# Kernel tuning notes

Measured on AMD Instinct MI355X. Metric: run time of the kernel, lower is better.

The kernel has to match this reference:

```python
import jax, jax.numpy as jnp
import numpy as np

MAX_WAVELENGTH = 10000
BIG_NEG = -2.3819763e38


def _apply_rope(x, positions):
    """RoPE: positions [B,L] applied to x [B,L,H,D]."""
    d = x.shape[-1]
    freq_exponents = (2.0 / d) * jnp.arange(d // 2, dtype=jnp.float32)
    timescale = MAX_WAVELENGTH ** freq_exponents  # [D/2]
    radians = positions[..., None].astype(jnp.float32) / timescale  # [B,L,D/2]
    radians = radians[..., None, :]  # [B,L,1,D/2]
    sin, cos = jnp.sin(radians), jnp.cos(radians)
    x1, x2 = jnp.split(x, 2, axis=-1)
    return jnp.concatenate([x1 * cos - x2 * sin, x2 * cos + x1 * sin], axis=-1)


def setup_inputs() -> dict:
    key = jax.random.key(0)
    B, S, D, N, K, H = 2, 2048, 2048, 8, 1, 256  # batch, seq, features, q heads, kv heads, head_dim
    k1, k2, k3, k4 = jax.random.split(key, 4)
    x = jax.random.normal(k1, (B, S, D), dtype=jnp.float32)
    positions = jnp.broadcast_to(jnp.arange(S, dtype=jnp.int32), (B, S))
    attn_mask = jnp.tril(jnp.ones((S, S), dtype=bool))[None, None].repeat(B, axis=0)  # causal [B,1,S,S]
    q_w = jax.random.normal(k2, (N, D, H), dtype=jnp.float32) * (D ** -0.5)      # lecun_normal in_axis=-2
    kv_w = jax.random.normal(k3, (2, K, D, H), dtype=jnp.float32) * (D ** -0.5)
    out_w = jax.random.normal(k4, (N, H, D), dtype=jnp.float32) * (H ** -0.5)
    return {"x": x, "positions": positions, "attn_mask": attn_mask,
            "q_w": q_w, "kv_w": kv_w, "out_w": out_w}


def reference(x, positions, attn_mask, q_w, kv_w, out_w):
    B, T, D = x.shape
    N, _, H = q_w.shape
    K = kv_w.shape[1]
    G = N // K
    dtype = x.dtype

    q = jnp.einsum('btd,ndh->btnh', x, q_w)          # [B,T,N,H]
    kv = jnp.einsum('bsd,ckdh->cbskh', x, kv_w)      # [2,B,S,K,H]
    k, v = kv[0], kv[1]

    q = _apply_rope(q, positions) * (H ** -0.5)
    k = _apply_rope(k, positions)

    # prefill path: cache_size == S, so cache == k, v; idx = S
    qg = q.reshape(B, T, K, G, H)
    logits = jnp.einsum('btkgh,bskh->bkgts', qg, k,
                        preferred_element_type=jnp.float32)  # [B,K,G,T,S] fp32
    masked = jnp.where(attn_mask[:, :, None, :, :], logits, BIG_NEG)
    probs = jax.nn.softmax(masked, axis=-1).astype(dtype)
    enc = jnp.einsum('bkgts,bskh->btkgh', probs, v).reshape(B, T, N, H)
    out = jnp.einsum('btnh,nhd->btd', enc, out_w)
    return out
```

## Files before the change

### kernel.cpp

```cpp
#include <hip/hip_runtime.h>
#include <hip/hip_bf16.h>
#include <stdint.h>

#define BB 2
#define SS 2048
#define DD 2048
#define NHEAD 8
#define HH 256

typedef __bf16 bf16_t;
typedef __bf16 bf16x8 __attribute__((ext_vector_type(8)));
typedef __bf16 bf16x4v __attribute__((ext_vector_type(4)));
typedef __bf16 bf16x2v __attribute__((ext_vector_type(2)));
typedef float f32x4 __attribute__((ext_vector_type(4)));
typedef float f32x16 __attribute__((ext_vector_type(16)));
typedef unsigned int u32;

__device__ static inline void gload_lds16(const void* g, void* l) {
  __builtin_amdgcn_global_load_lds(
      (__attribute__((address_space(1))) void*)(g),
      (__attribute__((address_space(3))) void*)(l), 16, 0, 0);
}

__device__ static inline u32 pk2(float a, float b) {
  bf16x2v t = {(bf16_t)a, (bf16_t)b};
  return __builtin_bit_cast(u32, t);
}

__global__ void cvt_x_kernel(const float* __restrict__ x, bf16_t* __restrict__ xb) {
  size_t i = ((size_t)blockIdx.x * 256 + threadIdx.x) * 4;
  float4 v = *(const float4*)(x + i);
  bf16x4v o = {(bf16_t)v.x, (bf16_t)v.y, (bf16_t)v.z, (bf16_t)v.w};
  *(bf16x4v*)(xb + i) = o;
}

__global__ void transpose_cvt(const float* __restrict__ in, bf16_t* __restrict__ out,
                              int R, int C) {
  __shared__ float tile[32][33];
  int bx = blockIdx.x, by = blockIdx.y, z = blockIdx.z;
  in  += (size_t)z * R * C;
  out += (size_t)z * R * C;
  int tx = threadIdx.x & 31, ty = threadIdx.x >> 5;
#pragma unroll
  for (int k = 0; k < 4; ++k) {
    int r = by * 32 + ty + k * 8, c = bx * 32 + tx;
    tile[ty + k * 8][tx] = in[(size_t)r * C + c];
  }
  __syncthreads();
#pragma unroll
  for (int k = 0; k < 4; ++k) {
    int c = bx * 32 + ty + k * 8, r = by * 32 + tx;
    out[(size_t)c * R + r] = (bf16_t)tile[tx][ty + k * 8];
  }
}

template <int OUT_F32>
__global__ __launch_bounds__(256) void gemm2b(const bf16_t* __restrict__ A,
                                              const bf16_t* __restrict__ BT,
                                              void* __restrict__ C,
                                              int M, int Nc, int Kd) {
  __shared__ __attribute__((aligned(16))) char LDS[81920];
  char* Abuf = LDS;
  char* Bbuf = LDS + 49152;
  const int ntiles = Nc >> 7;
  int nwg = gridDim.x;
  int bid = ((nwg & 7) == 0) ? ((blockIdx.x & 7) * (nwg >> 3) + (blockIdx.x >> 3))
                             : blockIdx.x;
  int mt = bid / ntiles, ntb = bid % ntiles;
  int t = threadIdx.x, lane = t & 63, w = t >> 6;
  int wm = w >> 1, wn = w & 1;
  int l15 = lane & 15, lg = lane >> 4;
  int srow = t >> 3;
  int scolb = ((t & 7) * 16) ^ ((srow & 7) << 4);
  const bf16_t* Asrc = A + (size_t)(mt * 128 + srow) * Kd + (scolb >> 1);
  const bf16_t* Bsrc = BT + (size_t)(ntb * 128 + srow) * Kd + (scolb >> 1);
  const int nkt = Kd >> 6;
  f32x4 acc[4][4] = {};

#define STAGE_A(kt_)                                                  \
  {                                                                   \
    char* d_ = Abuf + ((kt_) % 3) * 16384 + t * 16;                   \
    const bf16_t* s_ = Asrc + (kt_)*64;                               \
    gload_lds16(s_, d_);                                              \
    gload_lds16(s_ + (size_t)32 * Kd, d_ + 4096);                     \
    gload_lds16(s_ + (size_t)64 * Kd, d_ + 8192);                     \
    gload_lds16(s_ + (size_t)96 * Kd, d_ + 12288);                    \
  }
#define STAGE_B(kt_)                                                  \
  {                                                                   \
    char* d_ = Bbuf + ((kt_)&1) * 16384 + t * 16;                     \
    const bf16_t* s_ = Bsrc + (kt_)*64;                               \
    gload_lds16(s_, d_);                                              \
    gload_lds16(s_ + (size_t)32 * Kd, d_ + 4096);                     \
    gload_lds16(s_ + (size_t)64 * Kd, d_ + 8192);                     \
    gload_lds16(s_ + (size_t)96 * Kd, d_ + 12288);                    \
  }

  STAGE_A(0);
  STAGE_B(0);
  STAGE_A(1);
  asm volatile("s_waitcnt vmcnt(4)" ::: "memory");
  __builtin_amdgcn_s_barrier();
  asm volatile("" ::: "memory");
  for (int kt = 0; kt < nkt; ++kt) {
    if (kt + 1 < nkt) STAGE_B(kt + 1);
    if (kt + 2 < nkt) STAGE_A(kt + 2);
    const char* Ab = Abuf + (kt % 3) * 16384;
    const char* Bb = Bbuf + (kt & 1) * 16384;
    int swz = (l15 & 7) << 4;
#pragma unroll
    for (int ks = 0; ks < 2; ++ks) {
      bf16x8 af[4], bfr[4];
#pragma unroll
      for (int i = 0; i < 4; ++i)
        af[i] = *(const bf16x8*)(Ab + (wm * 64 + i * 16 + l15) * 128 +
                                 ((ks * 64 + lg * 16) ^ swz));
#pragma unroll
      for (int j = 0; j < 4; ++j)
        bfr[j] = *(const bf16x8*)(Bb + (wn * 64 + j * 16 + l15) * 128 +
                                  ((ks * 64 + lg * 16) ^ swz));
      __builtin_amdgcn_s_setprio(1);
#pragma unroll
      for (int i = 0; i < 4; ++i)
#pragma unroll
        for (int j = 0; j < 4; ++j)
          acc[i][j] = __builtin_amdgcn_mfma_f32_16x16x32_bf16(af[i], bfr[j], acc[i][j], 0, 0, 0);
      __builtin_amdgcn_s_setprio(0);
    }
    if (kt + 1 < nkt) {
      if (kt + 2 < nkt) {
        asm volatile("s_waitcnt vmcnt(4)" ::: "memory");
      } else {
        asm volatile("s_waitcnt vmcnt(0)" ::: "memory");
      }
      __builtin_amdgcn_s_barrier();
      asm volatile("" ::: "memory");
    }
  }
#undef STAGE_A
#undef STAGE_B
#pragma unroll
  for (int i = 0; i < 4; ++i)
#pragma unroll
    for (int j = 0; j < 4; ++j) {
      int row = mt * 128 + wm * 64 + i * 16 + lg * 4;
      int col = ntb * 128 + wn * 64 + j * 16 + l15;
#pragma unroll
      for (int v = 0; v < 4; ++v) {
        if (OUT_F32)
          ((float*)C)[(size_t)(row + v) * Nc + col] = acc[i][j][v];
        else
          ((bf16_t*)C)[(size_t)(row + v) * Nc + col] = (bf16_t)acc[i][j][v];
      }
    }
}

__global__ void rope_kernel(bf16_t* __restrict__ qkv, const int* __restrict__ positions) {
  int idx = blockIdx.x * 256 + threadIdx.x;
  const int QP = 4096 * 8 * 16;
  int i0, row;
  bf16_t* p1;
  float scl;
  if (idx < QP) {
    i0 = (idx & 15) * 8;
    int nh = (idx >> 4) & 7;
    row = idx >> 7;
    p1 = qkv + (size_t)row * 2560 + nh * 256 + i0;
    scl = 0.0625f;
  } else {
    int kk = idx - QP;
    i0 = (kk & 15) * 8;
    row = kk >> 4;
    p1 = qkv + (size_t)row * 2560 + 2048 + i0;
    scl = 1.0f;
  }
  float pos = (float)positions[row];
  bf16x8 v1 = *(const bf16x8*)p1;
  bf16x8 v2 = *(const bf16x8*)(p1 + 128);
  bf16x8 o1, o2;
#pragma unroll
  for (int j = 0; j < 8; ++j) {
    float ang = pos * __expf(-(float)(i0 + j) * (9.2103403719761836f / 128.f));
    float s = __sinf(ang), c = __cosf(ang);
    float x1 = (float)v1[j], x2 = (float)v2[j];
    o1[j] = (bf16_t)((x1 * c - x2 * s) * scl);
    o2[j] = (bf16_t)((x2 * c + x1 * s) * scl);
  }
  *(bf16x8*)p1 = o1;
  *(bf16x8*)(p1 + 128) = o2;
}

__global__ void vt_kernel(const bf16_t* __restrict__ qkv, bf16_t* __restrict__ vt) {
  __shared__ bf16_t tile[32][34];
  int bx = blockIdx.x;
  int by = blockIdx.y;
  int b = blockIdx.z;
  int tx = threadIdx.x & 31, ty = threadIdx.x >> 5;
#pragma unroll
  for (int k = 0; k < 4; ++k) {
    int s = bx * 32 + ty + k * 8, h = by * 32 + tx;
    tile[ty + k * 8][tx] = qkv[((size_t)(b * SS + s)) * 2560 + 2304 + h];
  }
  __syncthreads();
#pragma unroll
  for (int k = 0; k < 4; ++k) {
    int h = by * 32 + ty + k * 8, s = bx * 32 + tx;
    vt[((size_t)(b * HH + h)) * 2048 + s] = tile[tx][ty + k * 8];
  }
}

__global__ __launch_bounds__(512)
void flash_kernel(const bf16_t* __restrict__ qkv, const bf16_t* __restrict__ vtg,
                  bf16_t* __restrict__ enc, u32* __restrict__ ctr) {
  __shared__ __attribute__((aligned(16))) char LDSRAW[149504];
  char* Kl = LDSRAW;
  char* Vl = LDSRAW + 65536;
  char* Pl = LDSRAW + 131072;
  float* lsumL = (float*)(LDSRAW + 147456);
  u32* slot = (u32*)(LDSRAW + 148992);
  int t = threadIdx.x, lane = t & 63, w = t >> 6;
  int l31 = lane & 31, h5 = lane >> 5;
  bool isQK = (w < 4);
  int wq = isQK ? (w & 1) : ((w - 4) & 1);
  int sh = (w >> 1) & 1;
  int hh = ((w - 4) >> 1) & 1;
  int rk0 = t >> 5;
  int cbk = ((t & 31) * 16) ^ ((rk0 & 15) << 4);
  int rv0 = t >> 3;
  int cbv = ((t & 7) * 16) ^ ((rv0 & 7) << 4);

  for (;;) {
    if (t == 0) *slot = atomicAdd(ctr, 1);
    __syncthreads();
    u32 ti = *slot;
    if (ti >= 512u) break;
    int qt = 31 - (int)(ti >> 4);
    int b = (int)(ti >> 3) & 1, n = (int)ti & 7;
    const bf16_t* kbase = qkv + (size_t)(b * SS) * 2560 + 2048;
    int qmin = qt * 64 + wq * 32;
    int q_g = qmin + l31;
    bf16x8 qf[16];
    if (isQK) {
      const bf16_t* qrow = qkv + ((size_t)(b * SS + q_g)) * 2560 + n * 256 + h5 * 8;
#pragma unroll
      for (int i = 0; i < 16; ++i) qf[i] = *(const bf16x8*)(qrow + i * 16);
    }
    f32x16 accO[4] = {};
    float l_r = 0.f;
#pragma unroll
    for (int r = 0; r < 4; ++r)
      gload_lds16(kbase + (size_t)(rk0 + 16 * r) * 2560 + (cbk >> 1), Kl + t * 16 + r * 8192);
    __syncthreads();
    for (int kt = 0; kt <= qt + 1; ++kt) {
      int cur = kt & 1, prv = cur ^ 1;
      if (kt <= qt) {
#pragma unroll
        for (int r = 0; r < 4; ++r)
          gload_lds16(vtg + ((size_t)(b * HH + rv0 + 64 * r)) * 2048 + kt * 64 + (cbv >> 1),
                      Vl + cur * 32768 + t * 16 + r * 8192);
      }
      if (kt < qt) {
#pragma unroll
        for (int r = 0; r < 4; ++r)
          gload_lds16(kbase + (size_t)((kt + 1) * 64 + rk0 + 16 * r) * 2560 + (cbk >> 1),
                      Kl + prv * 32768 + t * 16 + r * 8192);
      }
      bool act = isQK && (kt <= qt) && (kt * 64 + sh * 32 <= qmin + 31);
      bool pact = (!isQK) && (kt >= 1);
      if (act) {
        const char* Kc = Kl + cur * 32768;
        int krow = sh * 32 + l31;
        int kswz = (l31 & 15) << 4;
        f32x16 scA = {}, scB = {};
        __builtin_amdgcn_s_setprio(1);
#pragma unroll
        for (int i = 0; i < 8; ++i) {
          bf16x8 kfa = *(const bf16x8*)(Kc + krow * 512 + (((2 * i) * 32 + h5 * 16) ^ kswz));
          bf16x8 kfb = *(const bf16x8*)(Kc + krow * 512 + (((2 * i + 1) * 32 + h5 * 16) ^ kswz));
          scA = __builtin_amdgcn_mfma_f32_32x32x16_bf16(kfa, qf[2 * i], scA, 0, 0, 0);
          scB = __builtin_amdgcn_mfma_f32_32x32x16_bf16(kfb, qf[2 * i + 1], scB, 0, 0, 0);
        }
        __builtin_amdgcn_s_setprio(0);
        f32x16 sc = scA + scB;
        int smin = kt * 64 + sh * 32;
        if (smin + 31 > qmin) {
#pragma unroll
          for (int r = 0; r < 16; ++r) {
            int s_g = smin + ((r & 3) + 8 * (r >> 2) + 4 * h5);
            if (s_g > q_g) sc[r] = -1e30f;
          }
        }
        float rs = 0.f;
#pragma unroll
        for (int r = 0; r < 16; ++r) {
          float p = __expf(sc[r] - 8.f);
          sc[r] = p;
          rs += p;
        }
        rs += __shfl_xor(rs, 32);
        l_r += rs;
        u32 u0 = pk2(sc[0], sc[1]),  u1 = pk2(sc[2], sc[3]);
        u32 u2 = pk2(sc[4], sc[5]),  u3 = pk2(sc[6], sc[7]);
        u32 u4 = pk2(sc[8], sc[9]),  u5 = pk2(sc[10], sc[11]);
        u32 u6 = pk2(sc[12], sc[13]), u7 = pk2(sc[14], sc[15]);
        u32 x0 = __shfl_xor(u0, 32), x1 = __shfl_xor(u1, 32);
        u32 x2 = __shfl_xor(u2, 32), x3 = __shfl_xor(u3, 32);
        u32 x4 = __shfl_xor(u4, 32), x5 = __shfl_xor(u5, 32);
        u32 x6 = __shfl_xor(u6, 32), x7 = __shfl_xor(u7, 32);
        union { u32 wd[4]; bf16x8 v; } f0, f1;
        f0.wd[0] = h5 ? x2 : u0;  f0.wd[1] = h5 ? x3 : u1;
        f0.wd[2] = h5 ? u2 : x0;  f0.wd[3] = h5 ? u3 : x1;
        f1.wd[0] = h5 ? x6 : u4;  f1.wd[1] = h5 ? x7 : u5;
        f1.wd[2] = h5 ? u6 : x4;  f1.wd[3] = h5 ? u7 : x5;
        char* Pw = Pl + cur * 8192 + wq * 4096;
        int pswz = (l31 & 7) << 4;
        *(bf16x8*)(Pw + l31 * 128 + ((sh * 64 + h5 * 16) ^ pswz)) = f0.v;
        *(bf16x8*)(Pw + l31 * 128 + ((sh * 64 + 32 + h5 * 16) ^ pswz)) = f1.v;
      }
      if (pact) {
        const char* Pw = Pl + prv * 8192 + wq * 4096;
        const char* Vc = Vl + prv * 32768;
        int pswz = (l31 & 7) << 4;
        int jmax = ((kt - 1 < qt) || wq == 1) ? 4 : 2;
        __builtin_amdgcn_s_setprio(1);
        for (int j = 0; j < jmax; ++j) {
          bf16x8 pf = *(const bf16x8*)(Pw + l31 * 128 + ((j * 32 + h5 * 16) ^ pswz));
#pragma unroll
          for (int ht = 0; ht < 4; ++ht) {
            int vrow = hh * 128 + ht * 32 + l31;
            bf16x8 vf = *(const bf16x8*)(Vc + vrow * 128 + ((j * 32 + h5 * 16) ^ pswz));
            accO[ht] = __builtin_amdgcn_mfma_f32_32x32x16_bf16(pf, vf, accO[ht], 0, 0, 0);
          }
        }
        __builtin_amdgcn_s_setprio(0);
      }
      __syncthreads();
    }
    if (isQK && h5 == 0) lsumL[sh * 64 + wq * 32 + l31] = l_r;
    __syncthreads();
    if (!isQK) {
      float lt = lsumL[wq * 32 + l31] + lsumL[64 + wq * 32 + l31];
      float rinv = 1.f / lt;
      float riv[16];
#pragma unroll
      for (int r = 0; r < 16; ++r) riv[r] = __shfl(rinv, (r & 3) + 8 * (r >> 2) + 4 * h5);
#pragma unroll
      for (int ht = 0; ht < 4; ++ht)
#pragma unroll
        for (int r = 0; r < 16; ++r) {
          int ql = (r & 3) + 8 * (r >> 2) + 4 * h5;
          enc[((size_t)(b * SS + qmin + ql)) * 2048 + n * 256 + hh * 128 + ht * 32 + l31] =
              (bf16_t)(accO[ht][r] * riv[r]);
        }
    }
    __syncthreads();
  }
}

extern "C" void kernel_launch(void* const* d_in, const int* in_sizes, int n_in,
                              void* d_out, int out_size, void* d_ws, size_t ws_size,
                              hipStream_t stream) {
  const float* x = (const float*)d_in[0];
  const int* positions = (const int*)d_in[1];
  const float* qw = (const float*)d_in[3];
  const float* kvw = (const float*)d_in[4];
  const float* outw = (const float*)d_in[5];

  char* ws = (char*)d_ws;
  if (ws_size < (size_t)75497472) return;
  bf16_t* xb      = (bf16_t*)(ws);
  bf16_t* qkvwbt  = (bf16_t*)(ws + 16777216);
  bf16_t* outwbt  = (bf16_t*)(ws + 27262976);
  bf16_t* qkvb    = (bf16_t*)(ws + 35651584);
  bf16_t* vtg     = (bf16_t*)(ws + 56623104);
  bf16_t* encb    = (bf16_t*)(ws + 58720256);
  u32* ctr        = (u32*)(ws);

  cvt_x_kernel<<<8192, 256, 0, stream>>>(x, xb);
  transpose_cvt<<<dim3(8, 64, 8), 256, 0, stream>>>(qw, qkvwbt, 2048, 256);
  transpose_cvt<<<dim3(8, 64, 2), 256, 0, stream>>>(kvw, qkvwbt + (size_t)2048 * 2048, 2048, 256);
  transpose_cvt<<<dim3(64, 64, 1), 256, 0, stream>>>(outw, outwbt, 2048, 2048);
  gemm2b<0><<<640, 256, 0, stream>>>(xb, qkvwbt, qkvb, 4096, 2560, 2048);
  rope_kernel<<<2304, 256, 0, stream>>>(qkvb, positions);
  vt_kernel<<<dim3(64, 8, 2), 256, 0, stream>>>(qkvb, vtg);
  hipMemsetAsync(ctr, 0, 4, stream);
  flash_kernel<<<256, 512, 0, stream>>>(qkvb, vtg, encb, ctr);
  gemm2b<1><<<512, 256, 0, stream>>>(encb, outwbt, d_out, 4096, 2048, 2048);
}
```

Measured before the change: 187.6 us.

## Stage Q in LDS and stream K/V tiles directly into registers

Q is now loaded once per tile into LDS, and K and V fragments are loaded straight from global memory into per-wave registers. The next K tile is prefetched in two halves between the MFMA halves, and V is prefetched for the next iteration. This drops the double-buffered K/V LDS staging and cuts LDS use from about 146KB to 96KB, removing LDS write/read traffic for K and V. In exchange each wave issues uncoalesced-ish global loads with no cross-wave sharing, so both QK waves with the same sh load the same K rows. Register pressure also rises.

```diff
diff --git a/kernel.cpp b/kernel.cpp
--- a/kernel.cpp
+++ b/kernel.cpp
@@ -212,22 +212,17 @@
 __global__ __launch_bounds__(512)
 void flash_kernel(const bf16_t* __restrict__ qkv, const bf16_t* __restrict__ vtg,
                   bf16_t* __restrict__ enc, u32* __restrict__ ctr) {
-  __shared__ __attribute__((aligned(16))) char LDSRAW[149504];
-  char* Kl = LDSRAW;
-  char* Vl = LDSRAW + 65536;
-  char* Pl = LDSRAW + 131072;
-  float* lsumL = (float*)(LDSRAW + 147456);
-  u32* slot = (u32*)(LDSRAW + 148992);
+  __shared__ __attribute__((aligned(16))) char LDSRAW[98304];
+  char* Ql = LDSRAW;
+  char* Pl = LDSRAW + 32768;
+  float* lsumL = (float*)(LDSRAW + 49152);
+  u32* slot = (u32*)(LDSRAW + 50176);
   int t = threadIdx.x, lane = t & 63, w = t >> 6;
   int l31 = lane & 31, h5 = lane >> 5;
   bool isQK = (w < 4);
   int wq = isQK ? (w & 1) : ((w - 4) & 1);
   int sh = (w >> 1) & 1;
   int hh = ((w - 4) >> 1) & 1;
-  int rk0 = t >> 5;
-  int cbk = ((t & 31) * 16) ^ ((rk0 & 15) << 4);
-  int rv0 = t >> 3;
-  int cbv = ((t & 7) * 16) ^ ((rv0 & 7) << 4);
 
   for (;;) {
     if (t == 0) *slot = atomicAdd(ctr, 1);
@@ -239,100 +234,127 @@
     const bf16_t* kbase = qkv + (size_t)(b * SS) * 2560 + 2048;
     int qmin = qt * 64 + wq * 32;
     int q_g = qmin + l31;
-    bf16x8 qf[16];
+    bf16x8 reg16[16];
+#pragma unroll
+    for (int r = 0; r < 4; ++r) {
+      int qrow = (t >> 5) + 16 * r;
+      int cb = ((t & 31) * 16) ^ ((qrow & 15) << 4);
+      gload_lds16(qkv + ((size_t)(b * SS + qt * 64 + qrow)) * 2560 + n * 256 + (cb >> 1),
+                  Ql + t * 16 + r * 8192);
+    }
     if (isQK) {
-      const bf16_t* qrow = qkv + ((size_t)(b * SS + q_g)) * 2560 + n * 256 + h5 * 8;
-#pragma unroll
-      for (int i = 0; i < 16; ++i) qf[i] = *(const bf16x8*)(qrow + i * 16);
+      const bf16_t* ks = kbase + (size_t)(sh * 32 + l31) * 2560 + h5 * 8;
+#pragma unroll
+      for (int i = 0; i < 16; ++i) reg16[i] = *(const bf16x8*)(ks + i * 16);
     }
     f32x16 accO[4] = {};
     float l_r = 0.f;
-#pragma unroll
-    for (int r = 0; r < 4; ++r)
-      gload_lds16(kbase + (size_t)(rk0 + 16 * r) * 2560 + (cbk >> 1), Kl + t * 16 + r * 8192);
     __syncthreads();
     for (int kt = 0; kt <= qt + 1; ++kt) {
       int cur = kt & 1, prv = cur ^ 1;
-      if (kt <= qt) {
-#pragma unroll
-        for (int r = 0; r < 4; ++r)
-          gload_lds16(vtg + ((size_t)(b * HH + rv0 + 64 * r)) * 2048 + kt * 64 + (cbv >> 1),
-                      Vl + cur * 32768 + t * 16 + r * 8192);
-      }
-      if (kt < qt) {
-#pragma unroll
-        for (int r = 0; r < 4; ++r)
-          gload_lds16(kbase + (size_t)((kt + 1) * 64 + rk0 + 16 * r) * 2560 + (cbk >> 1),
-                      Kl + prv * 32768 + t * 16 + r * 8192);
-      }
       bool act = isQK && (kt <= qt) && (kt * 64 + sh * 32 <= qmin + 31);
-      bool pact = (!isQK) && (kt >= 1);
-      if (act) {
-        const char* Kc = Kl + cur * 32768;
-        int krow = sh * 32 + l31;
-        int kswz = (l31 & 15) << 4;
+      if (isQK) {
         f32x16 scA = {}, scB = {};
-        __builtin_amdgcn_s_setprio(1);
-#pragma unroll
-        for (int i = 0; i < 8; ++i) {
-          bf16x8 kfa = *(const bf16x8*)(Kc + krow * 512 + (((2 * i) * 32 + h5 * 16) ^ kswz));
-          bf16x8 kfb = *(const bf16x8*)(Kc + krow * 512 + (((2 * i + 1) * 32 + h5 * 16) ^ kswz));
-          scA = __builtin_amdgcn_mfma_f32_32x32x16_bf16(kfa, qf[2 * i], scA, 0, 0, 0);
-          scB = __builtin_amdgcn_mfma_f32_32x32x16_bf16(kfb, qf[2 * i + 1], scB, 0, 0, 0);
-        }
-        __builtin_amdgcn_s_setprio(0);
-        f32x16 sc = scA + scB;
-        int smin = kt * 64 + sh * 32;
-        if (smin + 31 > qmin) {
+        int qrow = wq * 32 + l31;
+        int qswz = (l31 & 15) << 4;
+        if (act) {
+          __builtin_amdgcn_s_setprio(1);
+#pragma unroll
+          for (int i = 0; i < 8; ++i) {
+            bf16x8 qv = *(const bf16x8*)(Ql + qrow * 512 + ((i * 32 + h5 * 16) ^ qswz));
+            if (i & 1)
+              scB = __builtin_amdgcn_mfma_f32_32x32x16_bf16(reg16[i], qv, scB, 0, 0, 0);
+            else
+              scA = __builtin_amdgcn_mfma_f32_32x32x16_bf16(reg16[i], qv, scA, 0, 0, 0);
+          }
+          __builtin_amdgcn_s_setprio(0);
+        }
+        if (kt < qt) {
+          const bf16_t* ks = kbase + (size_t)((kt + 1) * 64 + sh * 32 + l31) * 2560 + h5 * 8;
+#pragma unroll
+          for (int i = 0; i < 8; ++i) reg16[i] = *(const bf16x8*)(ks + i * 16);
+        }
+        if (act) {
+          __builtin_amdgcn_s_setprio(1);
+#pragma unroll
+          for (int i = 8; i < 16; ++i) {
+            bf16x8 qv = *(const bf16x8*)(Ql + qrow * 512 + ((i * 32 + h5 * 16) ^ qswz));
+            if (i & 1)
+              scB = __builtin_amdgcn_mfma_f32_32x32x16_bf16(reg16[i], qv, scB, 0, 0, 0);
+            else
+              scA = __builtin_amdgcn_mfma_f32_32x32x16_bf16(reg16[i], qv, scA, 0, 0, 0);
+          }
+          __builtin_amdgcn_s_setprio(0);
+        }
+        if (kt < qt) {
+          const bf16_t* ks = kbase + (size_t)((kt + 1) * 64 + sh * 32 + l31) * 2560 + h5 * 8;
+#pragma unroll
+          for (int i = 8; i < 16; ++i) reg16[i] = *(const bf16x8*)(ks + i * 16);
+        }
+        if (act) {
+          f32x16 sc = scA + scB;
+          int smin = kt * 64 + sh * 32;
+          if (smin + 31 > qmin) {
+#pragma unroll
+            for (int r = 0; r < 16; ++r) {
+              int s_g = smin + ((r & 3) + 8 * (r >> 2) + 4 * h5);
+              if (s_g > q_g) sc[r] = -1e30f;
+            }
+          }
+          float rs = 0.f;
 #pragma unroll
           for (int r = 0; r < 16; ++r) {
-            int s_g = smin + ((r & 3) + 8 * (r >> 2) + 4 * h5);
-            if (s_g > q_g) sc[r] = -1e30f;
+            float p = __expf(sc[r] - 8.f);
+            sc[r] = p;
+            rs += p;
           }
-        }
-        float rs = 0.f;
-#pragma unroll
-        for (int r = 0; r < 16; ++r) {
-          float p = __expf(sc[r] - 8.f);
-          sc[r] = p;
-          rs += p;
-        }
-        rs += __shfl_xor(rs, 32);
-        l_r += rs;
-        u32 u0 = pk2(sc[0], sc[1]),  u1 = pk2(sc[2], sc[3]);
-        u32 u2 = pk2(sc[4], sc[5]),  u3 = pk2(sc[6], sc[7]);
-        u32 u4 = pk2(sc[8], sc[9]),  u5 = pk2(sc[10], sc[11]);
-        u32 u6 = pk2(sc[12], sc[13]), u7 = pk2(sc[14], sc[15]);
-        u32 x0 = __shfl_xor(u0, 32), x1 = __shfl_xor(u1, 32);
-        u32 x2 = __shfl_xor(u2, 32), x3 = __shfl_xor(u3, 32);
-        u32 x4 = __shfl_xor(u4, 32), x5 = __shfl_xor(u5, 32);
-        u32 x6 = __shfl_xor(u6, 32), x7 = __shfl_xor(u7, 32);
-        union { u32 wd[4]; bf16x8 v; } f0, f1;
-        f0.wd[0] = h5 ? x2 : u0;  f0.wd[1] = h5 ? x3 : u1;
-        f0.wd[2] = h5 ? u2 : x0;  f0.wd[3] = h5 ? u3 : x1;
-        f1.wd[0] = h5 ? x6 : u4;  f1.wd[1] = h5 ? x7 : u5;
-        f1.wd[2] = h5 ? u6 : x4;  f1.wd[3] = h5 ? u7 : x5;
-        char* Pw = Pl + cur * 8192 + wq * 4096;
-        int pswz = (l31 & 7) << 4;
-        *(bf16x8*)(Pw + l31 * 128 + ((sh * 64 + h5 * 16) ^ pswz)) = f0.v;
-        *(bf16x8*)(Pw + l31 * 128 + ((sh * 64 + 32 + h5 * 16) ^ pswz)) = f1.v;
-      }
-      if (pact) {
-        const char* Pw = Pl + prv * 8192 + wq * 4096;
-        const char* Vc = Vl + prv * 32768;
-        int pswz = (l31 & 7) << 4;
-        int jmax = ((kt - 1 < qt) || wq == 1) ? 4 : 2;
-        __builtin_amdgcn_s_setprio(1);
-        for (int j = 0; j < jmax; ++j) {
-          bf16x8 pf = *(const bf16x8*)(Pw + l31 * 128 + ((j * 32 + h5 * 16) ^ pswz));
-#pragma unroll
-          for (int ht = 0; ht < 4; ++ht) {
-            int vrow = hh * 128 + ht * 32 + l31;
-            bf16x8 vf = *(const bf16x8*)(Vc + vrow * 128 + ((j * 32 + h5 * 16) ^ pswz));
-            accO[ht] = __builtin_amdgcn_mfma_f32_32x32x16_bf16(pf, vf, accO[ht], 0, 0, 0);
+          rs += __shfl_xor(rs, 32);
+          l_r += rs;
+          u32 u0 = pk2(sc[0], sc[1]),  u1 = pk2(sc[2], sc[3]);
+          u32 u2 = pk2(sc[4], sc[5]),  u3 = pk2(sc[6], sc[7]);
+          u32 u4 = pk2(sc[8], sc[9]),  u5 = pk2(sc[10], sc[11]);
+          u32 u6 = pk2(sc[12], sc[13]), u7 = pk2(sc[14], sc[15]);
+          u32 x0 = __shfl_xor(u0, 32), x1 = __shfl_xor(u1, 32);
+          u32 x2 = __shfl_xor(u2, 32), x3 = __shfl_xor(u3, 32);
+          u32 x4 = __shfl_xor(u4, 32), x5 = __shfl_xor(u5, 32);
+          u32 x6 = __shfl_xor(u6, 32), x7 = __shfl_xor(u7, 32);
+          union { u32 wd[4]; bf16x8 v; } f0, f1;
+          f0.wd[0] = h5 ? x2 : u0;  f0.wd[1] = h5 ? x3 : u1;
+          f0.wd[2] = h5 ? u2 : x0;  f0.wd[3] = h5 ? u3 : x1;
+          f1.wd[0] = h5 ? x6 : u4;  f1.wd[1] = h5 ? x7 : u5;
+          f1.wd[2] = h5 ? u6 : x4;  f1.wd[3] = h5 ? u7 : x5;
+          char* Pw = Pl + cur * 8192 + wq * 4096;
+          int pswz = (l31 & 7) << 4;
+          *(bf16x8*)(Pw + l31 * 128 + ((sh * 64 + h5 * 16) ^ pswz)) = f0.v;
+          *(bf16x8*)(Pw + l31 * 128 + ((sh * 64 + 32 + h5 * 16) ^ pswz)) = f1.v;
+        }
+      } else {
+        if (kt >= 1) {
+          const char* Pw = Pl + prv * 8192 + wq * 4096;
+          int pswz = (l31 & 7) << 4;
+          int jmax = ((kt - 1 < qt) || wq == 1) ? 4 : 2;
+          __builtin_amdgcn_s_setprio(1);
+#pragma unroll
+          for (int j = 0; j < 4; ++j) {
+            if (j < jmax) {
+              bf16x8 pf = *(const bf16x8*)(Pw + l31 * 128 + ((j * 32 + h5 * 16) ^ pswz));
+#pragma unroll
+              for (int ht = 0; ht < 4; ++ht)
+                accO[ht] =
+                    __builtin_amdgcn_mfma_f32_32x32x16_bf16(pf, reg16[ht * 4 + j], accO[ht], 0, 0, 0);
+            }
           }
-        }
-        __builtin_amdgcn_s_setprio(0);
+          __builtin_amdgcn_s_setprio(0);
+        }
+        if (kt <= qt) {
+          const bf16_t* vs =
+              vtg + ((size_t)(b * HH + hh * 128 + l31)) * 2048 + kt * 64 + h5 * 8;
+#pragma unroll
+          for (int ht = 0; ht < 4; ++ht)
+#pragma unroll
+            for (int j = 0; j < 4; ++j)
+              reg16[ht * 4 + j] = *(const bf16x8*)(vs + (size_t)(ht * 32) * 2048 + j * 16);
+        }
       }
       __syncthreads();
     }
```

New measurement: 252.5 us. 34.6% more time.
